# Kernel optimization log

Hardware: AMD Instinct MI355X
Metric: run time of the kernel (lower is better)

## Reference

```python
import jax, jax.numpy as jnp
import numpy as np

N_NODES = 20000
STEPS = 10  # message_passing_steps


def _mlp(x, p):
    # 3-layer MLP: Linear->ReLU->Linear->ReLU->Linear (no final activation)
    W1, b1, W2, b2, W3, b3 = p
    h = jax.nn.relu(x @ W1 + b1)
    h = jax.nn.relu(h @ W2 + b2)
    return h @ W3 + b3


def _aggregate(dst, edge_attr, num_nodes):
    # scatter_add of edge features into destination nodes, degree-normalized (deg clamped to >=1)
    agg = jax.ops.segment_sum(edge_attr, dst, num_segments=num_nodes)
    deg = jax.ops.segment_sum(jnp.ones((dst.shape[0], 1), edge_attr.dtype), dst, num_segments=num_nodes)
    return agg / jnp.maximum(deg, 1.0)


def setup_inputs() -> dict:
    key = jax.random.key(0)
    N, EM, EC = N_NODES, 120000, 20000
    ND, MD, CD, OD, L = 12, 7, 4, 3, 128
    keys = iter(jax.random.split(key, 128))

    def lin(i, o):
        return (jax.random.normal(next(keys), (i, o), jnp.float32) * 0.05,
                jax.random.normal(next(keys), (o,), jnp.float32) * 0.05)

    inp = {
        "node_x": jax.random.normal(next(keys), (N, ND), jnp.float32),
        "mesh_edge_attr": jax.random.normal(next(keys), (EM, MD), jnp.float32),
        "contact_edge_attr": jax.random.normal(next(keys), (EC, CD), jnp.float32),
    }
    dims = {"ne": (ND, L), "me": (MD, L), "ce": (CD, L), "pe": (3 * L, L), "pn": (3 * L, L), "de": (L, OD)}
    for name, (i, o) in dims.items():
        W1, b1 = lin(i, L)
        W2, b2 = lin(L, L)
        W3, b3 = lin(L, o)
        for pn, p in zip(["W1", "b1", "W2", "b2", "W3", "b3"], [W1, b1, W2, b2, W3, b3]):
            inp[name + "_" + pn] = p
    inp["mesh_edge_index"] = jax.random.randint(next(keys), (2, EM), 0, N)
    inp["contact_edge_index"] = jax.random.randint(next(keys), (2, EC), 0, N)
    return inp


def reference(node_x, mesh_edge_attr, contact_edge_attr,
              ne_W1, ne_b1, ne_W2, ne_b2, ne_W3, ne_b3,
              me_W1, me_b1, me_W2, me_b2, me_W3, me_b3,
              ce_W1, ce_b1, ce_W2, ce_b2, ce_W3, ce_b3,
              pe_W1, pe_b1, pe_W2, pe_b2, pe_W3, pe_b3,
              pn_W1, pn_b1, pn_W2, pn_b2, pn_W3, pn_b3,
              de_W1, de_b1, de_W2, de_b2, de_W3, de_b3,
              mesh_edge_index, contact_edge_index):
    ne = (ne_W1, ne_b1, ne_W2, ne_b2, ne_W3, ne_b3)
    mep = (me_W1, me_b1, me_W2, me_b2, me_W3, me_b3)
    cep = (ce_W1, ce_b1, ce_W2, ce_b2, ce_W3, ce_b3)
    pe = (pe_W1, pe_b1, pe_W2, pe_b2, pe_W3, pe_b3)
    pn = (pn_W1, pn_b1, pn_W2, pn_b2, pn_W3, pn_b3)
    de = (de_W1, de_b1, de_W2, de_b2, de_W3, de_b3)
    N = node_x.shape[0]
    # encode
    x = _mlp(node_x, ne)                 # [N, 128]
    me = _mlp(mesh_edge_attr, mep)       # [EM, 128]
    ce = _mlp(contact_edge_attr, cep)    # [EC, 128]
    msrc, mdst = mesh_edge_index[0], mesh_edge_index[1]
    csrc, cdst = contact_edge_index[0], contact_edge_index[1]
    # process (shared edge_mlp for both edge types, residual updates)
    for _ in range(STEPS):
        me = me + _mlp(jnp.concatenate([x[msrc], x[mdst], me], axis=-1), pe)
        ce = ce + _mlp(jnp.concatenate([x[csrc], x[cdst], ce], axis=-1), pe)
        agg_m = _aggregate(mdst, me, N)
        agg_c = _aggregate(cdst, ce, N)
        x = x + _mlp(jnp.concatenate([x, agg_m, agg_c], axis=-1), pn)
    # decode
    return _mlp(x, de)                   # [N, 3]
```

## Files before the change

kernel.cpp:

```cpp
#include <hip/hip_runtime.h>
#include <stdint.h>

typedef unsigned short u16;
typedef __attribute__((ext_vector_type(8))) short bf16x8;
typedef __attribute__((ext_vector_type(4))) float f32x4;

#define NNODES 20000
#define EM 120000
#define EC 20000
#define LDIM 128
#define MT 32
#define MT2 64
#define A_STR 392
#define H_STR 136
#define G_STR 264
#define D_STR 132

__device__ __forceinline__ u16 f2bf(float f){
  uint32_t b = __float_as_uint(f);
  b += 0x7FFF + ((b >> 16) & 1);
  return (u16)(b >> 16);
}

__device__ __forceinline__ f32x4 mfma16(bf16x8 a, bf16x8 b, f32x4 c){
  return __builtin_amdgcn_mfma_f32_16x16x32_bf16(a, b, c, 0, 0, 0);
}

template<int KB>
__device__ __forceinline__ void layer(const u16* sIn, int in_str, const u16* Wp,
                                      int wr, int wc, int lane, f32x4 acc[4]){
  const int row = wr*16 + (lane & 15);
  const int kg  = lane >> 4;
  #pragma unroll
  for (int kb = 0; kb < KB; ++kb){
    bf16x8 a = *(const bf16x8*)(sIn + row*in_str + kb*32 + kg*8);
    const u16* wb = Wp + (((kb*8 + wc*4)*64 + lane) << 3);
    #pragma unroll
    for (int nf = 0; nf < 4; ++nf){
      bf16x8 b = *(const bf16x8*)(wb + (nf << 9));
      acc[nf] = mfma16(a, b, acc[nf]);
    }
  }
}

__device__ __forceinline__ void hid_epi(f32x4 acc[4], const float* bias,
                                        int wr, int wc, int lane, u16* sOut){
  const int cl = lane & 15;
  const int r0 = wr*16 + (lane >> 4)*4;
  #pragma unroll
  for (int nf = 0; nf < 4; ++nf){
    int col = wc*64 + nf*16 + cl;
    float bv = bias[col];
    #pragma unroll
    for (int r = 0; r < 4; ++r){
      float v = acc[nf][r] + bv;
      sOut[(r0 + r)*H_STR + col] = f2bf(v > 0.f ? v : 0.f);
    }
  }
}

__device__ __forceinline__ void zero4(f32x4 acc[4]){
  const f32x4 vz = {0.f, 0.f, 0.f, 0.f};
  #pragma unroll
  for (int i = 0; i < 4; ++i) acc[i] = vz;
}

template<int KB, int STR>
__device__ __forceinline__ void layer64(const u16* sIn, const u16* Wp,
                                        int wr, int wc, int lane, f32x4 acc[2][2]){
  const int r0 = wr*32 + (lane & 15);
  const int kg = lane >> 4;
  const u16* a0p = sIn + r0*STR + kg*8;
  const u16* a1p = a0p + 16*STR;
  const u16* wb  = Wp + (((wc*2)*64 + lane) << 3);
  #pragma unroll
  for (int kb = 0; kb < KB; ++kb){
    bf16x8 a0 = *(const bf16x8*)(a0p + kb*32);
    bf16x8 a1 = *(const bf16x8*)(a1p + kb*32);
    const u16* wk = wb + kb*4096;
    bf16x8 b0 = *(const bf16x8*)(wk);
    bf16x8 b1 = *(const bf16x8*)(wk + 512);
    acc[0][0] = mfma16(a0, b0, acc[0][0]);
    acc[1][0] = mfma16(a1, b0, acc[1][0]);
    acc[0][1] = mfma16(a0, b1, acc[0][1]);
    acc[1][1] = mfma16(a1, b1, acc[1][1]);
  }
}

template<int STR>
__device__ __forceinline__ void hid_epi64(f32x4 acc[2][2], const float* bias,
                                          int wr, int wc, int lane, u16* sOut){
  const int cl = lane & 15;
  const int rq = (lane >> 4)*4;
  #pragma unroll
  for (int rf = 0; rf < 2; ++rf){
    int r0 = wr*32 + rf*16 + rq;
    #pragma unroll
    for (int nf = 0; nf < 2; ++nf){
      int col = wc*32 + nf*16 + cl;
      float bv = bias[col];
      #pragma unroll
      for (int r = 0; r < 4; ++r){
        float v = acc[rf][nf][r] + bv;
        sOut[(r0 + r)*STR + col] = f2bf(v > 0.f ? v : 0.f);
      }
    }
  }
}

__device__ __forceinline__ void zero22(f32x4 acc[2][2]){
  const f32x4 vz = {0.f, 0.f, 0.f, 0.f};
  acc[0][0] = vz; acc[0][1] = vz; acc[1][0] = vz; acc[1][1] = vz;
}

struct PackDesc { const float* src; int K_raw, N_raw, NF, elem_off; };
struct PackArgs { PackDesc d[18]; int total; };

__global__ __launch_bounds__(256) void pack_weights(PackArgs pa, u16* dst){
  int idx = blockIdx.x*256 + threadIdx.x;
  if (idx >= pa.total) return;
  int di = 0;
  #pragma unroll
  for (int i = 1; i < 18; ++i) if (idx >= pa.d[i].elem_off) di = i;
  PackDesc dd = pa.d[di];
  int e = idx - dd.elem_off;
  int f = e >> 9, lane = (e >> 3) & 63, j = e & 7;
  int kb = f / dd.NF, nf = f % dd.NF;
  int k = kb*32 + (lane >> 4)*8 + j;
  int n = nf*16 + (lane & 15);
  float v = (k < dd.K_raw && n < dd.N_raw) ? dd.src[k*dd.N_raw + n] : 0.f;
  dst[idx] = f2bf(v);
}

__global__ __launch_bounds__(256) void hist_kernel(const int* mdst, const int* cdst,
                                                   int* cnt_m, int* cnt_c){
  int i = blockIdx.x*256 + threadIdx.x;
  if (i < EM) atomicAdd(&cnt_m[mdst[i]], 1);
  else if (i < EM + EC) atomicAdd(&cnt_c[cdst[i - EM]], 1);
}

struct ScanArgs { const int *cnt_m, *cnt_c; int *start_m, *start_c, *cur_m, *cur_c; };

__global__ __launch_bounds__(256) void scan_kernel(ScanArgs a){
  const int n = NNODES;
  const int* cnt = blockIdx.x == 0 ? a.cnt_m : a.cnt_c;
  int* start     = blockIdx.x == 0 ? a.start_m : a.start_c;
  int* cur       = blockIdx.x == 0 ? a.cur_m : a.cur_c;
  __shared__ int part[256];
  __shared__ int base[257];
  int t = threadIdx.x;
  const int per = (n + 255) / 256;
  int lo = t*per, hi = min(n, lo + per);
  int s = 0;
  for (int j = lo; j < hi; ++j) s += cnt[j];
  part[t] = s;
  __syncthreads();
  if (t == 0){
    int run = 0;
    for (int i = 0; i < 256; ++i){ base[i] = run; run += part[i]; }
    base[256] = run;
  }
  __syncthreads();
  int run = base[t];
  for (int j = lo; j < hi; ++j){ start[j] = run; cur[j] = run; run += cnt[j]; }
  if (t == 255) start[n] = base[256];
}

__global__ __launch_bounds__(256) void scatter_kernel(const int* mdst, const int* cdst,
                                                      int* cur_m, int* cur_c,
                                                      int* eid_m, int* eid_c){
  int i = blockIdx.x*256 + threadIdx.x;
  if (i < EM){
    int p = atomicAdd(&cur_m[mdst[i]], 1);
    eid_m[p] = i;
  } else if (i < EM + EC){
    int e = i - EM;
    int p = atomicAdd(&cur_c[cdst[e]], 1);
    eid_c[p] = e;
  }
}

struct EncArgs {
  const float* in; int Kraw;
  const u16 *Wp1, *Wp2, *Wp3;
  const float *b1, *b2, *b3;
  float* out_f32; u16* out_b16;
};

__global__ __launch_bounds__(256) void enc_kernel(EncArgs a){
  __shared__ u16 sA[MT*A_STR];
  __shared__ u16 sH[MT*H_STR];
  const int tid = threadIdx.x, lane = tid & 63, w = tid >> 6, wr = w & 1, wc = w >> 1;
  const int m0 = blockIdx.x * MT;
  for (int i = tid; i < MT*32; i += 256){
    int row = i >> 5, c = i & 31;
    float v = (c < a.Kraw) ? a.in[(size_t)(m0 + row)*a.Kraw + c] : 0.f;
    sA[row*A_STR + c] = f2bf(v);
  }
  __syncthreads();
  f32x4 acc[4]; zero4(acc);
  layer<1>(sA, A_STR, a.Wp1, wr, wc, lane, acc);
  hid_epi(acc, a.b1, wr, wc, lane, sH);
  __syncthreads();
  zero4(acc);
  layer<4>(sH, H_STR, a.Wp2, wr, wc, lane, acc);
  hid_epi(acc, a.b2, wr, wc, lane, sA);
  __syncthreads();
  zero4(acc);
  layer<4>(sA, H_STR, a.Wp3, wr, wc, lane, acc);
  const int cl = lane & 15, r0l = wr*16 + (lane >> 4)*4;
  #pragma unroll
  for (int nf = 0; nf < 4; ++nf){
    int col = wc*64 + nf*16 + cl;
    float bv = a.b3[col];
    #pragma unroll
    for (int r = 0; r < 4; ++r){
      int m = m0 + r0l + r;
      float v = acc[nf][r] + bv;
      a.out_f32[(size_t)m*LDIM + col] = v;
      if (a.out_b16) a.out_b16[(size_t)m*LDIM + col] = f2bf(v);
    }
  }
}

struct EdgeArgs {
  const u16 *Wp1, *Wp2, *Wp3;
  const float *b1, *b2, *b3;
  const u16* x_b16;
  const int *msrc, *mdst, *csrc, *cdst;
  float *me_f32, *ce_f32;
  int mesh_blocks;
};

__global__ __launch_bounds__(512, 6) void edge_kernel(EdgeArgs a){
  __shared__ u16 sCat[MT2*A_STR];
  const int tid = threadIdx.x, lane = tid & 63, w = tid >> 6, wr = w & 1, wc = w >> 1;
  const bool mesh = (int)blockIdx.x < a.mesh_blocks;
  const int e0 = (mesh ? (int)blockIdx.x : (int)blockIdx.x - a.mesh_blocks) * MT2;
  const int E = mesh ? EM : EC;
  const int* src = mesh ? a.msrc : a.csrc;
  const int* dst = mesh ? a.mdst : a.cdst;
  float* ff = mesh ? a.me_f32 : a.ce_f32;

  #pragma unroll
  for (int i = tid; i < MT2*32; i += 512){
    int row = i >> 5, c = i & 31;
    int e = e0 + row; if (e >= E) e = E - 1;
    const u16* sp = (c < 16) ? a.x_b16 + (size_t)src[e]*LDIM + c*8
                             : a.x_b16 + (size_t)dst[e]*LDIM + (c-16)*8;
    *(bf16x8*)(sCat + row*A_STR + c*8) = *(const bf16x8*)sp;
  }
  const int srow = tid >> 3, sj = tid & 7;
  int se = e0 + srow; if (se >= E) se = E - 1;
  const f32x4* fp = (const f32x4*)(ff + (size_t)se*LDIM + sj*16);
  f32x4 p0 = fp[0], p1 = fp[1], p2 = fp[2], p3 = fp[3];
  {
    bf16x8 t0, t1;
    #pragma unroll
    for (int k = 0; k < 4; ++k){
      t0[k] = (short)f2bf(p0[k]); t0[k+4] = (short)f2bf(p1[k]);
      t1[k] = (short)f2bf(p2[k]); t1[k+4] = (short)f2bf(p3[k]);
    }
    *(bf16x8*)(sCat + srow*A_STR + 256 + sj*16) = t0;
    *(bf16x8*)(sCat + srow*A_STR + 256 + sj*16 + 8) = t1;
  }
  __syncthreads();

  f32x4 acc[2][2]; zero22(acc);
  layer64<12, A_STR>(sCat, a.Wp1, wr, wc, lane, acc);
  __syncthreads();
  hid_epi64<A_STR>(acc, a.b1, wr, wc, lane, sCat + 256);
  __syncthreads();
  zero22(acc);
  layer64<4, A_STR>(sCat + 256, a.Wp2, wr, wc, lane, acc);
  hid_epi64<A_STR>(acc, a.b2, wr, wc, lane, sCat);
  __syncthreads();
  zero22(acc);
  layer64<4, A_STR>(sCat, a.Wp3, wr, wc, lane, acc);
  __syncthreads();

  float* dd = (float*)sCat;
  {
    const int cl = lane & 15, rq = (lane >> 4)*4;
    #pragma unroll
    for (int rf = 0; rf < 2; ++rf){
      #pragma unroll
      for (int nf = 0; nf < 2; ++nf){
        int col = wc*32 + nf*16 + cl;
        float bv = a.b3[col];
        #pragma unroll
        for (int r = 0; r < 4; ++r)
          dd[(wr*32 + rf*16 + rq + r)*D_STR + col] = acc[rf][nf][r] + bv;
      }
    }
  }
  __syncthreads();
  if (e0 + srow < E){
    float* op = ff + (size_t)(e0 + srow)*LDIM + sj*16;
    const f32x4* dp = (const f32x4*)(dd + srow*D_STR + sj*16);
    f32x4 n0 = p0 + dp[0], n1 = p1 + dp[1], n2 = p2 + dp[2], n3 = p3 + dp[3];
    ((f32x4*)op)[0] = n0; ((f32x4*)op)[1] = n1; ((f32x4*)op)[2] = n2; ((f32x4*)op)[3] = n3;
  }
}

struct NodeArgs {
  const u16 *Wp1, *Wp2, *Wp3;
  const float *b1, *b2, *b3;
  const u16* x_b16_in;
  const float *me_f32, *ce_f32;
  const int *start_m, *eid_m, *start_c, *eid_c;
  float* x_f32; u16* x_b16_out;
};

__global__ __launch_bounds__(512, 8) void node_kernel(NodeArgs a){
  __shared__ u16 sG[MT2*G_STR];
  const int tid = threadIdx.x, lane = tid & 63, w = tid >> 6, wr = w & 1, wc = w >> 1;
  const int n0 = blockIdx.x * MT2;

  {
    const int r = tid >> 3, c0 = (tid & 7) * 16;
    const int n = n0 + r;
    const bool ok = n < NNODES;
    {
      int s = ok ? a.start_m[n] : 0, e = ok ? a.start_m[n+1] : 0;
      f32x4 a0{0,0,0,0}, a1{0,0,0,0}, a2{0,0,0,0}, a3{0,0,0,0};
      for (int j = s; j < e; ++j){
        const f32x4* p = (const f32x4*)(a.me_f32 + (size_t)a.eid_m[j]*LDIM + c0);
        a0 += p[0]; a1 += p[1]; a2 += p[2]; a3 += p[3];
      }
      float inv = 1.f / fmaxf((float)(e - s), 1.f);
      bf16x8 t0, t1;
      #pragma unroll
      for (int k = 0; k < 4; ++k){
        t0[k]   = (short)f2bf(a0[k]*inv); t0[k+4] = (short)f2bf(a1[k]*inv);
        t1[k]   = (short)f2bf(a2[k]*inv); t1[k+4] = (short)f2bf(a3[k]*inv);
      }
      *(bf16x8*)(sG + r*G_STR + c0) = t0;
      *(bf16x8*)(sG + r*G_STR + c0 + 8) = t1;
    }
    {
      int s = ok ? a.start_c[n] : 0, e = ok ? a.start_c[n+1] : 0;
      f32x4 a0{0,0,0,0}, a1{0,0,0,0}, a2{0,0,0,0}, a3{0,0,0,0};
      for (int j = s; j < e; ++j){
        const f32x4* p = (const f32x4*)(a.ce_f32 + (size_t)a.eid_c[j]*LDIM + c0);
        a0 += p[0]; a1 += p[1]; a2 += p[2]; a3 += p[3];
      }
      float inv = 1.f / fmaxf((float)(e - s), 1.f);
      bf16x8 t0, t1;
      #pragma unroll
      for (int k = 0; k < 4; ++k){
        t0[k]   = (short)f2bf(a0[k]*inv); t0[k+4] = (short)f2bf(a1[k]*inv);
        t1[k]   = (short)f2bf(a2[k]*inv); t1[k+4] = (short)f2bf(a3[k]*inv);
      }
      *(bf16x8*)(sG + r*G_STR + 128 + c0) = t0;
      *(bf16x8*)(sG + r*G_STR + 128 + c0 + 8) = t1;
    }
  }
  __syncthreads();

  const int r0 = wr*32 + (lane & 15);
  int nA = n0 + r0;      if (nA >= NNODES) nA = NNODES - 1;
  int nB = n0 + r0 + 16; if (nB >= NNODES) nB = NNODES - 1;

  f32x4 acc[2][2]; zero22(acc);
  {
    const int cb = (lane >> 4)*8;
    const u16* wb = a.Wp1 + (((wc*2)*64 + lane) << 3);
    #pragma unroll
    for (int kb = 0; kb < 12; ++kb){
      bf16x8 a0, a1;
      if (kb < 4){
        a0 = *(const bf16x8*)(a.x_b16_in + (size_t)nA*LDIM + kb*32 + cb);
        a1 = *(const bf16x8*)(a.x_b16_in + (size_t)nB*LDIM + kb*32 + cb);
      } else {
        a0 = *(const bf16x8*)(sG + r0*G_STR + (kb-4)*32 + cb);
        a1 = *(const bf16x8*)(sG + (r0+16)*G_STR + (kb-4)*32 + cb);
      }
      const u16* wk = wb + kb*4096;
      bf16x8 b0 = *(const bf16x8*)(wk);
      bf16x8 b1 = *(const bf16x8*)(wk + 512);
      acc[0][0] = mfma16(a0, b0, acc[0][0]);
      acc[1][0] = mfma16(a1, b0, acc[1][0]);
      acc[0][1] = mfma16(a0, b1, acc[0][1]);
      acc[1][1] = mfma16(a1, b1, acc[1][1]);
    }
  }
  __syncthreads();
  hid_epi64<G_STR>(acc, a.b1, wr, wc, lane, sG);
  __syncthreads();
  zero22(acc);
  layer64<4, G_STR>(sG, a.Wp2, wr, wc, lane, acc);
  hid_epi64<G_STR>(acc, a.b2, wr, wc, lane, sG + 128);
  __syncthreads();
  zero22(acc);
  layer64<4, G_STR>(sG + 128, a.Wp3, wr, wc, lane, acc);

  const int cl = lane & 15, rq = (lane >> 4)*4;
  #pragma unroll
  for (int rf = 0; rf < 2; ++rf){
    #pragma unroll
    for (int r = 0; r < 4; ++r){
      int n = n0 + wr*32 + rf*16 + rq + r;
      if (n < NNODES){
        #pragma unroll
        for (int nf = 0; nf < 2; ++nf){
          int col = wc*32 + nf*16 + cl;
          float nv = a.x_f32[(size_t)n*LDIM + col] + acc[rf][nf][r] + a.b3[col];
          a.x_f32[(size_t)n*LDIM + col] = nv;
          a.x_b16_out[(size_t)n*LDIM + col] = f2bf(nv);
        }
      }
    }
  }
}

struct DecArgs {
  const u16 *Wp1, *Wp2, *Wp3;
  const float *b1, *b2, *b3;
  const u16* x_b16; float* out;
};

__global__ __launch_bounds__(256) void dec_kernel(DecArgs a){
  __shared__ u16 sA[MT*A_STR];
  __shared__ u16 sH[MT*H_STR];
  const int tid = threadIdx.x, lane = tid & 63, w = tid >> 6, wr = w & 1, wc = w >> 1;
  const int n0 = blockIdx.x * MT;
  for (int i = tid; i < MT*16; i += 256){
    int row = i >> 4, ch = i & 15;
    *(bf16x8*)(sA + row*H_STR + ch*8) = *(const bf16x8*)(a.x_b16 + (size_t)(n0+row)*LDIM + ch*8);
  }
  __syncthreads();
  f32x4 acc[4]; zero4(acc);
  layer<4>(sA, H_STR, a.Wp1, wr, wc, lane, acc);
  hid_epi(acc, a.b1, wr, wc, lane, sH);
  __syncthreads();
  zero4(acc);
  layer<4>(sH, H_STR, a.Wp2, wr, wc, lane, acc);
  hid_epi(acc, a.b2, wr, wc, lane, sA);
  __syncthreads();
  if (wc == 0){
    f32x4 a3 = {0.f, 0.f, 0.f, 0.f};
    const int row = wr*16 + (lane & 15), kg = lane >> 4;
    #pragma unroll
    for (int kb = 0; kb < 4; ++kb){
      bf16x8 av = *(const bf16x8*)(sA + row*H_STR + kb*32 + kg*8);
      bf16x8 bv = *(const bf16x8*)(a.Wp3 + ((kb*64 + lane) << 3));
      a3 = mfma16(av, bv, a3);
    }
    const int cl = lane & 15, r0l = wr*16 + (lane >> 4)*4;
    if (cl < 3){
      #pragma unroll
      for (int r = 0; r < 4; ++r)
        a.out[(size_t)(n0 + r0l + r)*3 + cl] = a3[r] + a.b3[cl];
    }
  }
}

extern "C" void kernel_launch(void* const* d_in, const int* in_sizes, int n_in,
                              void* d_out, int out_size, void* d_ws, size_t ws_size,
                              hipStream_t stream){
  auto F = [&](int i){ return (const float*)d_in[i]; };
  const float* node_x   = F(0);
  const float* mesh_attr = F(1);
  const float* cont_attr = F(2);
  const int* mei = (const int*)d_in[39];
  const int* cei = (const int*)d_in[40];
  const int *msrc = mei, *mdst = mei + EM, *csrc = cei, *cdst = cei + EC;

  char* ws = (char*)d_ws;
  size_t off = 0;
  auto take = [&](size_t b)->void*{ void* p = ws + off; off += (b + 255) & ~(size_t)255; return p; };
  float* x_f32  = (float*)take((size_t)NNODES*LDIM*4);
  u16*   x_b16  = (u16*)  take((size_t)NNODES*LDIM*2);
  float* me_f32 = (float*)take((size_t)EM*LDIM*4);
  float* ce_f32 = (float*)take((size_t)EC*LDIM*4);
  u16*   wpack  = (u16*)  take((size_t)309248*2);
  int* cnt_m   = (int*)take((size_t)NNODES*4);
  int* cnt_c   = (int*)take((size_t)NNODES*4);
  int* start_m = (int*)take((size_t)(NNODES+1)*4);
  int* start_c = (int*)take((size_t)(NNODES+1)*4);
  int* cur_m   = (int*)take((size_t)NNODES*4);
  int* cur_c   = (int*)take((size_t)NNODES*4);
  int* eid_m   = (int*)take((size_t)EM*4);
  int* eid_c   = (int*)take((size_t)EC*4);

  static const int tbl[18][5] = {
    {3,12,128,32,128},{5,128,128,128,128},{7,128,128,128,128},
    {9,7,128,32,128},{11,128,128,128,128},{13,128,128,128,128},
    {15,4,128,32,128},{17,128,128,128,128},{19,128,128,128,128},
    {21,384,128,384,128},{23,128,128,128,128},{25,128,128,128,128},
    {27,384,128,384,128},{29,128,128,128,128},{31,128,128,128,128},
    {33,128,128,128,128},{35,128,128,128,128},{37,128,3,128,16}};
  PackArgs pa; int eo = 0; int offs[18];
  for (int i = 0; i < 18; ++i){
    offs[i] = eo;
    pa.d[i].src = F(tbl[i][0]);
    pa.d[i].K_raw = tbl[i][1];
    pa.d[i].N_raw = tbl[i][2];
    pa.d[i].NF = tbl[i][4] / 16;
    pa.d[i].elem_off = eo;
    eo += tbl[i][3] * tbl[i][4];
  }
  pa.total = eo;
  pack_weights<<<dim3(eo/256), dim3(256), 0, stream>>>(pa, wpack);

  size_t cnt_span = ((char*)cnt_c - (char*)cnt_m) + (size_t)NNODES*4;
  hipMemsetAsync(cnt_m, 0, cnt_span, stream);
  hist_kernel<<<dim3((EM + EC + 255)/256), dim3(256), 0, stream>>>(mdst, cdst, cnt_m, cnt_c);
  ScanArgs sa{cnt_m, cnt_c, start_m, start_c, cur_m, cur_c};
  scan_kernel<<<dim3(2), dim3(256), 0, stream>>>(sa);
  scatter_kernel<<<dim3((EM + EC + 255)/256), dim3(256), 0, stream>>>(mdst, cdst, cur_m, cur_c, eid_m, eid_c);

  EncArgs en{node_x, 12, wpack+offs[0], wpack+offs[1], wpack+offs[2], F(4), F(6), F(8), x_f32, x_b16};
  enc_kernel<<<dim3(NNODES/MT), dim3(256), 0, stream>>>(en);
  EncArgs em{mesh_attr, 7, wpack+offs[3], wpack+offs[4], wpack+offs[5], F(10), F(12), F(14), me_f32, nullptr};
  enc_kernel<<<dim3(EM/MT), dim3(256), 0, stream>>>(em);
  EncArgs ec{cont_attr, 4, wpack+offs[6], wpack+offs[7], wpack+offs[8], F(16), F(18), F(20), ce_f32, nullptr};
  enc_kernel<<<dim3(EC/MT), dim3(256), 0, stream>>>(ec);

  EdgeArgs ea;
  ea.Wp1 = wpack+offs[9]; ea.Wp2 = wpack+offs[10]; ea.Wp3 = wpack+offs[11];
  ea.b1 = F(22); ea.b2 = F(24); ea.b3 = F(26);
  ea.x_b16 = x_b16;
  ea.msrc = msrc; ea.mdst = mdst; ea.csrc = csrc; ea.cdst = cdst;
  ea.me_f32 = me_f32; ea.ce_f32 = ce_f32;
  ea.mesh_blocks = EM/MT2;

  NodeArgs na;
  na.Wp1 = wpack+offs[12]; na.Wp2 = wpack+offs[13]; na.Wp3 = wpack+offs[14];
  na.b1 = F(28); na.b2 = F(30); na.b3 = F(32);
  na.x_b16_in = x_b16;
  na.me_f32 = me_f32; na.ce_f32 = ce_f32;
  na.start_m = start_m; na.eid_m = eid_m; na.start_c = start_c; na.eid_c = eid_c;
  na.x_f32 = x_f32; na.x_b16_out = x_b16;

  const int edge_blocks = EM/MT2 + (EC + MT2 - 1)/MT2;
  const int node_blocks = (NNODES + MT2 - 1)/MT2;
  for (int s = 0; s < 10; ++s){
    edge_kernel<<<dim3(edge_blocks), dim3(512), 0, stream>>>(ea);
    node_kernel<<<dim3(node_blocks), dim3(512), 0, stream>>>(na);
  }

  DecArgs da{wpack+offs[15], wpack+offs[16], wpack+offs[17], F(34), F(36), F(38), x_b16, (float*)d_out};
  dec_kernel<<<dim3(NNODES/MT), dim3(256), 0, stream>>>(da);
}
```

Before: 1.218 ms.

## Shrink node kernel tile to 32 rows for more blocks and parallel gather

The node-update kernel now processes 32 nodes per block instead of 64. That gives 625 blocks instead of 313, and each gather thread handles 8 feature columns instead of 16. The x tile is staged into shared memory alongside both aggregates, and the MLP layers run with a 16x32 per-wave MFMA tile. The goal is more parallelism and latency hiding in the irregular gather phase. The cost is halved weight reuse per block and a lower occupancy hint.

```diff
diff --git a/kernel.cpp b/kernel.cpp
--- a/kernel.cpp
+++ b/kernel.cpp
@@ -13,7 +13,6 @@
 #define MT2 64
 #define A_STR 392
 #define H_STR 136
-#define G_STR 264
 #define D_STR 132
 
 __device__ __forceinline__ u16 f2bf(float f){
@@ -111,6 +110,41 @@
 __device__ __forceinline__ void zero22(f32x4 acc[2][2]){
   const f32x4 vz = {0.f, 0.f, 0.f, 0.f};
   acc[0][0] = vz; acc[0][1] = vz; acc[1][0] = vz; acc[1][1] = vz;
+}
+
+template<int KB, int STR>
+__device__ __forceinline__ void layer32(const u16* sIn, const u16* Wp,
+                                        int wr, int wc, int lane, f32x4 acc[2]){
+  const int r0 = wr*16 + (lane & 15);
+  const int kg = lane >> 4;
+  const u16* a0p = sIn + r0*STR + kg*8;
+  const u16* wb  = Wp + (((wc*2)*64 + lane) << 3);
+  #pragma unroll
+  for (int kb = 0; kb < KB; ++kb){
+    bf16x8 a0 = *(const bf16x8*)(a0p + kb*32);
+    const u16* wk = wb + kb*4096;
+    bf16x8 b0 = *(const bf16x8*)(wk);
+    bf16x8 b1 = *(const bf16x8*)(wk + 512);
+    acc[0] = mfma16(a0, b0, acc[0]);
+    acc[1] = mfma16(a0, b1, acc[1]);
+  }
+}
+
+template<int STR>
+__device__ __forceinline__ void hid_epi32(f32x4 acc[2], const float* bias,
+                                          int wr, int wc, int lane, u16* sOut){
+  const int cl = lane & 15;
+  const int r0 = wr*16 + (lane >> 4)*4;
+  #pragma unroll
+  for (int nf = 0; nf < 2; ++nf){
+    int col = wc*32 + nf*16 + cl;
+    float bv = bias[col];
+    #pragma unroll
+    for (int r = 0; r < 4; ++r){
+      float v = acc[nf][r] + bv;
+      sOut[(r0 + r)*STR + col] = f2bf(v > 0.f ? v : 0.f);
+    }
+  }
 }
 
 struct PackDesc { const float* src; int K_raw, N_raw, NF, elem_off; };
@@ -312,104 +346,70 @@
   float* x_f32; u16* x_b16_out;
 };
 
-__global__ __launch_bounds__(512, 8) void node_kernel(NodeArgs a){
-  __shared__ u16 sG[MT2*G_STR];
+__global__ __launch_bounds__(512, 6) void node_kernel(NodeArgs a){
+  __shared__ u16 sA[MT*A_STR];
   const int tid = threadIdx.x, lane = tid & 63, w = tid >> 6, wr = w & 1, wc = w >> 1;
-  const int n0 = blockIdx.x * MT2;
+  const int n0 = blockIdx.x * MT;
 
   {
-    const int r = tid >> 3, c0 = (tid & 7) * 16;
+    int row = tid >> 4, ch = tid & 15;
+    *(bf16x8*)(sA + row*A_STR + ch*8) =
+        *(const bf16x8*)(a.x_b16_in + (size_t)(n0+row)*LDIM + ch*8);
+  }
+  {
+    const int r = tid >> 4, c0 = (tid & 15) * 8;
     const int n = n0 + r;
-    const bool ok = n < NNODES;
     {
-      int s = ok ? a.start_m[n] : 0, e = ok ? a.start_m[n+1] : 0;
-      f32x4 a0{0,0,0,0}, a1{0,0,0,0}, a2{0,0,0,0}, a3{0,0,0,0};
+      int s = a.start_m[n], e = a.start_m[n+1];
+      f32x4 a0{0,0,0,0}, a1{0,0,0,0};
       for (int j = s; j < e; ++j){
         const f32x4* p = (const f32x4*)(a.me_f32 + (size_t)a.eid_m[j]*LDIM + c0);
-        a0 += p[0]; a1 += p[1]; a2 += p[2]; a3 += p[3];
+        a0 += p[0]; a1 += p[1];
       }
       float inv = 1.f / fmaxf((float)(e - s), 1.f);
-      bf16x8 t0, t1;
+      bf16x8 t;
       #pragma unroll
-      for (int k = 0; k < 4; ++k){
-        t0[k]   = (short)f2bf(a0[k]*inv); t0[k+4] = (short)f2bf(a1[k]*inv);
-        t1[k]   = (short)f2bf(a2[k]*inv); t1[k+4] = (short)f2bf(a3[k]*inv);
-      }
-      *(bf16x8*)(sG + r*G_STR + c0) = t0;
-      *(bf16x8*)(sG + r*G_STR + c0 + 8) = t1;
+      for (int k = 0; k < 4; ++k){ t[k] = (short)f2bf(a0[k]*inv); t[k+4] = (short)f2bf(a1[k]*inv); }
+      *(bf16x8*)(sA + r*A_STR + 128 + c0) = t;
     }
     {
-      int s = ok ? a.start_c[n] : 0, e = ok ? a.start_c[n+1] : 0;
-      f32x4 a0{0,0,0,0}, a1{0,0,0,0}, a2{0,0,0,0}, a3{0,0,0,0};
+      int s = a.start_c[n], e = a.start_c[n+1];
+      f32x4 a0{0,0,0,0}, a1{0,0,0,0};
       for (int j = s; j < e; ++j){
         const f32x4* p = (const f32x4*)(a.ce_f32 + (size_t)a.eid_c[j]*LDIM + c0);
-        a0 += p[0]; a1 += p[1]; a2 += p[2]; a3 += p[3];
+        a0 += p[0]; a1 += p[1];
       }
       float inv = 1.f / fmaxf((float)(e - s), 1.f);
-      bf16x8 t0, t1;
+      bf16x8 t;
       #pragma unroll
-      for (int k = 0; k < 4; ++k){
-        t0[k]   = (short)f2bf(a0[k]*inv); t0[k+4] = (short)f2bf(a1[k]*inv);
-        t1[k]   = (short)f2bf(a2[k]*inv); t1[k+4] = (short)f2bf(a3[k]*inv);
-      }
-      *(bf16x8*)(sG + r*G_STR + 128 + c0) = t0;
-      *(bf16x8*)(sG + r*G_STR + 128 + c0 + 8) = t1;
-    }
-  }
-  __syncthreads();
-
-  const int r0 = wr*32 + (lane & 15);
-  int nA = n0 + r0;      if (nA >= NNODES) nA = NNODES - 1;
-  int nB = n0 + r0 + 16; if (nB >= NNODES) nB = NNODES - 1;
-
-  f32x4 acc[2][2]; zero22(acc);
-  {
-    const int cb = (lane >> 4)*8;
-    const u16* wb = a.Wp1 + (((wc*2)*64 + lane) << 3);
-    #pragma unroll
-    for (int kb = 0; kb < 12; ++kb){
-      bf16x8 a0, a1;
-      if (kb < 4){
-        a0 = *(const bf16x8*)(a.x_b16_in + (size_t)nA*LDIM + kb*32 + cb);
-        a1 = *(const bf16x8*)(a.x_b16_in + (size_t)nB*LDIM + kb*32 + cb);
-      } else {
-        a0 = *(const bf16x8*)(sG + r0*G_STR + (kb-4)*32 + cb);
-        a1 = *(const bf16x8*)(sG + (r0+16)*G_STR + (kb-4)*32 + cb);
-      }
-      const u16* wk = wb + kb*4096;
-      bf16x8 b0 = *(const bf16x8*)(wk);
-      bf16x8 b1 = *(const bf16x8*)(wk + 512);
-      acc[0][0] = mfma16(a0, b0, acc[0][0]);
-      acc[1][0] = mfma16(a1, b0, acc[1][0]);
-      acc[0][1] = mfma16(a0, b1, acc[0][1]);
-      acc[1][1] = mfma16(a1, b1, acc[1][1]);
-    }
-  }
-  __syncthreads();
-  hid_epi64<G_STR>(acc, a.b1, wr, wc, lane, sG);
-  __syncthreads();
-  zero22(acc);
-  layer64<4, G_STR>(sG, a.Wp2, wr, wc, lane, acc);
-  hid_epi64<G_STR>(acc, a.b2, wr, wc, lane, sG + 128);
-  __syncthreads();
-  zero22(acc);
-  layer64<4, G_STR>(sG + 128, a.Wp3, wr, wc, lane, acc);
+      for (int k = 0; k < 4; ++k){ t[k] = (short)f2bf(a0[k]*inv); t[k+4] = (short)f2bf(a1[k]*inv); }
+      *(bf16x8*)(sA + r*A_STR + 256 + c0) = t;
+    }
+  }
+  __syncthreads();
+
+  f32x4 acc[2]; acc[0] = f32x4{0,0,0,0}; acc[1] = f32x4{0,0,0,0};
+  layer32<12, A_STR>(sA, a.Wp1, wr, wc, lane, acc);
+  __syncthreads();
+  hid_epi32<A_STR>(acc, a.b1, wr, wc, lane, sA + 256);
+  __syncthreads();
+  acc[0] = f32x4{0,0,0,0}; acc[1] = f32x4{0,0,0,0};
+  layer32<4, A_STR>(sA + 256, a.Wp2, wr, wc, lane, acc);
+  hid_epi32<A_STR>(acc, a.b2, wr, wc, lane, sA);
+  __syncthreads();
+  acc[0] = f32x4{0,0,0,0}; acc[1] = f32x4{0,0,0,0};
+  layer32<4, A_STR>(sA, a.Wp3, wr, wc, lane, acc);
 
   const int cl = lane & 15, rq = (lane >> 4)*4;
   #pragma unroll
-  for (int rf = 0; rf < 2; ++rf){
-    #pragma unroll
-    for (int r = 0; r < 4; ++r){
-      int n = n0 + wr*32 + rf*16 + rq + r;
-      if (n < NNODES){
-        #pragma unroll
-        for (int nf = 0; nf < 2; ++nf){
-          int col = wc*32 + nf*16 + cl;
-          float nv = a.x_f32[(size_t)n*LDIM + col] + acc[rf][nf][r] + a.b3[col];
-          a.x_f32[(size_t)n*LDIM + col] = nv;
-          a.x_b16_out[(size_t)n*LDIM + col] = f2bf(nv);
-        }
-      }
+  for (int r = 0; r < 4; ++r){
+    int n = n0 + wr*16 + rq + r;
+    #pragma unroll
+    for (int nf = 0; nf < 2; ++nf){
+      int col = wc*32 + nf*16 + cl;
+      float nv = a.x_f32[(size_t)n*LDIM + col] + acc[nf][r] + a.b3[col];
+      a.x_f32[(size_t)n*LDIM + col] = nv;
+      a.x_b16_out[(size_t)n*LDIM + col] = f2bf(nv);
     }
   }
 }
@@ -535,7 +535,7 @@
   na.x_f32 = x_f32; na.x_b16_out = x_b16;
 
   const int edge_blocks = EM/MT2 + (EC + MT2 - 1)/MT2;
-  const int node_blocks = (NNODES + MT2 - 1)/MT2;
+  const int node_blocks = NNODES/MT;
   for (int s = 0; s < 10; ++s){
     edge_kernel<<<dim3(edge_blocks), dim3(512), 0, stream>>>(ea);
     node_kernel<<<dim3(node_blocks), dim3(512), 0, stream>>>(na);
```

Result: faster. 1.165 ms (-4.4%).
